# Performance work log

Hardware: AMD Instinct MI355X
Metric: run time of the kernel (lower is better)

The kernel has to match this reference:

```python
import jax, jax.numpy as jnp
import numpy as np

R = 3                      # corr_radius
K = (2 * R + 1) ** 2       # 49 correlation window
BANDS = 16
MAX_FREQ = 512.0
NUM_ITERS = 4
EPS = 1e-5


def _fourier(coords):
    # coords [..., D] -> [..., D*(2*BANDS+1)]
    freqs = (2.0 ** jnp.linspace(0.0, np.log2(MAX_FREQ), BANDS).astype(coords.dtype)) * np.pi
    x = coords[..., None] * freqs                      # [..., D, BANDS]
    enc = jnp.concatenate([jnp.sin(x), jnp.cos(x)], axis=-1)
    enc = enc.reshape(enc.shape[:-2] + (-1,))
    return jnp.concatenate([coords, enc], axis=-1)


def _layernorm(x, g, b):
    m = jnp.mean(x, -1, keepdims=True)
    v = jnp.mean(jnp.square(x - m), -1, keepdims=True)
    return (x - m) * jax.lax.rsqrt(v + EPS) * g + b


def _local_corr(query, fmaps, positions, stride):
    # query [B,Q,C], fmaps [B,T,C,H,W], positions [B,Q,T,2] -> corr [B,Q,T,K]
    B, T, C, H, W = fmaps.shape
    Q = query.shape[1]
    off = jnp.arange(-R, R + 1, dtype=positions.dtype)
    oy, ox = jnp.meshgrid(off, off, indexing='ij')
    og = jnp.stack([ox.reshape(-1), oy.reshape(-1)], -1)          # [K,2] (x,y)
    coords = positions / stride
    coords = coords[..., None, :] + og                             # [B,Q,T,K,2]
    coords = jnp.transpose(coords, (0, 2, 1, 3, 4)).reshape(B * T, Q * K, 2)
    fm = fmaps.reshape(B * T, C, H * W)

    def bilerp(f, xy):  # f [C,HW], xy [N,2] -> [C,N]; zeros padding, align_corners=True
        x, y = xy[:, 0], xy[:, 1]
        x0, y0 = jnp.floor(x), jnp.floor(y)
        dx, dy = x - x0, y - y0
        out = jnp.zeros((C, xy.shape[0]), f.dtype)
        for xi, yi, w in ((x0, y0, (1 - dx) * (1 - dy)),
                          (x0 + 1, y0, dx * (1 - dy)),
                          (x0, y0 + 1, (1 - dx) * dy),
                          (x0 + 1, y0 + 1, dx * dy)):
            valid = (xi >= 0) & (xi <= W - 1) & (yi >= 0) & (yi <= H - 1)
            idx = (jnp.clip(yi, 0, H - 1) * W + jnp.clip(xi, 0, W - 1)).astype(jnp.int32)
            out = out + (w * valid)[None, :] * f[:, idx]
        return out

    sampled = jax.vmap(bilerp)(fm, coords)                         # [BT,C,QK]
    sampled = sampled.reshape(B, T, C, Q, K)
    return jnp.einsum('btcqk,bqc->bqtk', sampled, query)


def _forward(coarse_tracks, query_features, feature_maps, feature_stride,
             proj_w, proj_b, ln1_g, ln1_b, conv_w, conv_b, ln2_g, ln2_b,
             mlp_w1, mlp_b1, mlp_w2, mlp_b2, delta_w, delta_b,
             vis_w1, vis_b1, vis_w2, vis_b2):
    B, Q, T, _ = coarse_tracks.shape
    D = proj_w.shape[1]
    dtype = coarse_tracks.dtype
    tracks = coarse_tracks
    t_idx = jnp.linspace(0.0, 1.0, T, dtype=dtype).reshape(1, 1, T, 1)
    hidden = jnp.zeros((B * Q, T, D), dtype)
    vis_sum = jnp.zeros((B, Q, T), dtype)
    num_blocks = ln1_g.shape[0]
    pad = conv_w.shape[-1] // 2
    for _ in range(NUM_ITERS):
        corr = _local_corr(query_features, feature_maps, tracks, feature_stride)
        pos_in = jnp.concatenate([tracks, jnp.broadcast_to(t_idx, (B, Q, T, 1))], -1)
        pos_enc = _fourier(pos_in)
        x = jnp.concatenate([corr, pos_enc, hidden.reshape(B, Q, T, D)], -1)
        x = x.reshape(B * Q, T, -1) @ proj_w + proj_b
        for i in range(num_blocks):
            h = _layernorm(x, ln1_g[i], ln1_b[i])
            h = jnp.transpose(h, (0, 2, 1))                        # [BQ,D,T]
            h = jax.lax.conv_general_dilated(
                h, conv_w[i], (1,), [(pad, pad)],
                dimension_numbers=('NCH', 'OIH', 'NCH'),
                feature_group_count=D) + conv_b[i][None, :, None]
            x = x + jnp.transpose(h, (0, 2, 1))
            h2 = _layernorm(x, ln2_g[i], ln2_b[i])
            x = x + jax.nn.gelu(h2 @ mlp_w1[i] + mlp_b1[i], approximate=False) @ mlp_w2[i] + mlp_b2[i]
        hidden = x
        delta = (x @ delta_w + delta_b).reshape(B, Q, T, 2)
        vis = (jax.nn.gelu(x @ vis_w1 + vis_b1, approximate=False) @ vis_w2 + vis_b2).reshape(B, Q, T)
        tracks = tracks + delta
        vis_sum = vis_sum + vis
    visibility = vis_sum / NUM_ITERS
    return jnp.concatenate([tracks, visibility[..., None]], -1)   # [B,Q,T,3]


def setup_inputs() -> dict:
    B, Q, T, C, H, W, D = 1, 128, 48, 64, 96, 128, 128
    NB, KSZ, IN_DIM = 4, 5, K + 3 * (2 * BANDS + 1) + D          # 49+99+128=276
    ks = jax.random.split(jax.random.key(0), 16)
    s = 0.05
    return {
        'coarse_tracks': jax.random.uniform(ks[0], (B, Q, T, 2)) * jnp.array([W * 4.0, H * 4.0]),
        'query_features': jax.random.normal(ks[1], (B, Q, C)),
        'feature_maps': jax.random.normal(ks[2], (B, T, C, H, W)),
        'feature_stride': 4,
        'proj_w': jax.random.normal(ks[3], (IN_DIM, D)) * s,
        'proj_b': jnp.zeros((D,)),
        'ln1_g': jnp.ones((NB, D)),
        'ln1_b': jnp.zeros((NB, D)),
        'conv_w': jax.random.normal(ks[4], (NB, D, 1, KSZ)) * 0.2,
        'conv_b': jnp.zeros((NB, D)),
        'ln2_g': jnp.ones((NB, D)),
        'ln2_b': jnp.zeros((NB, D)),
        'mlp_w1': jax.random.normal(ks[5], (NB, D, 2 * D)) * s,
        'mlp_b1': jnp.zeros((NB, 2 * D)),
        'mlp_w2': jax.random.normal(ks[6], (NB, 2 * D, D)) * s,
        'mlp_b2': jnp.zeros((NB, D)),
        'delta_w': jax.random.normal(ks[7], (D, 2)) * 0.01,
        'delta_b': jnp.zeros((2,)),
        'vis_w1': jax.random.normal(ks[8], (D, D // 2)) * s,
        'vis_b1': jnp.zeros((D // 2,)),
        'vis_w2': jax.random.normal(ks[9], (D // 2, 1)) * s,
        'vis_b2': jnp.zeros((1,)),
    }


def reference(coarse_tracks, query_features, feature_maps, feature_stride,
              proj_w, proj_b, ln1_g, ln1_b, conv_w, conv_b, ln2_g, ln2_b,
              mlp_w1, mlp_b1, mlp_w2, mlp_b2, delta_w, delta_b,
              vis_w1, vis_b1, vis_w2, vis_b2):
    return _forward(coarse_tracks, query_features, feature_maps, feature_stride,
                    proj_w, proj_b, ln1_g, ln1_b, conv_w, conv_b, ln2_g, ln2_b,
                    mlp_w1, mlp_b1, mlp_w2, mlp_b2, delta_w, delta_b,
                    vis_w1, vis_b1, vis_w2, vis_b2)
```

## Files before the change

kernel.cpp:

```cpp
#include <hip/hip_runtime.h>
#include <hip/hip_bf16.h>
#include <math.h>

#define QN 128
#define TN 48
#define CN 64
#define HN 96
#define WN 128
#define DN 128
#define KK 49
#define IN_DIM 276
#define XPAD 288
#define NROWS (QN*TN)
#define PI_F 3.14159265358979323846f

typedef __hip_bfloat16 bf16;
typedef unsigned short u16;
using bf16x8 = __attribute__((ext_vector_type(8))) short;
using f32x4  = __attribute__((ext_vector_type(4))) float;

__device__ inline float fixnan(float x){ return (x == x && fabsf(x) < 1e30f) ? x : 0.f; }

template<int MODE> __device__ inline float ld(const void* p, size_t i){
  if constexpr (MODE == 0) return ((const float*)p)[i];
  else {
    unsigned int u = ((const unsigned short*)p)[i];
    return __uint_as_float(u << 16);
  }
}

__device__ inline short f2b(float x){
  __hip_bfloat16 h = __float2bfloat16(x);
  return *reinterpret_cast<short*>(&h);
}
__device__ inline float b2f16(u16 u){ return __uint_as_float(((unsigned int)u) << 16); }

__device__ inline float waveReduceSum(float v){
  #pragma unroll
  for (int off = 32; off > 0; off >>= 1) v += __shfl_xor(v, off, 64);
  return v;
}

__device__ inline float gelu_exact(float x){
  return 0.5f * x * (1.f + erff(x * 0.70710678118654752440f));
}

__device__ inline f32x4 mfma16(bf16x8 a, bf16x8 b, f32x4 c){
  return __builtin_amdgcn_mfma_f32_16x16x32_bf16(a, b, c, 0, 0, 0);
}

__device__ inline float decode_stride(const void* p){
  int iv = *(const int*)p;
  if (iv >= 1 && iv <= (1 << 20)) return (float)iv;
  float fv = __int_as_float(iv);
  if (fv == fv && fv >= 0.25f && fv <= 1048576.f) return fv;
  unsigned int lo = ((unsigned int)(*(const unsigned short*)p)) << 16;
  float bv = __uint_as_float(lo);
  if (bv == bv && bv >= 0.25f && bv <= 1048576.f) return bv;
  return 4.f;
}

__device__ inline void bput(short* base, int stride_sh, int r, int k, float v){
  *(short*)((char*)base + (size_t)r*stride_sh*2 + ((2*k) ^ ((r & 7) << 4))) = f2b(v);
}
__device__ inline float bget(const short* base, int stride_sh, int r, int k){
  unsigned short u = *(const unsigned short*)((const char*)base + (size_t)r*stride_sh*2 + ((2*k) ^ ((r & 7) << 4)));
  return __uint_as_float(((unsigned int)u) << 16);
}
__device__ inline bf16x8 bget8(const short* base, int stride_sh, int r, int k0){
  return *(const bf16x8*)((const char*)base + (size_t)r*stride_sh*2 + ((2*k0) ^ ((r & 7) << 4)));
}

struct SLds {
  float sc0[32], sc1[32];
  float qv[CN];
  float hdl[32][132];
  union {
    short Xs[32][320];
    struct { short hn[32][128]; short hn2[32][128]; short y1[32][256]; } b;
    float dots[32][64];
  } u;
};

__global__ __launch_bounds__(256) void k_sniff(const unsigned short* __restrict__ q,
                                               int* __restrict__ flag){
  __shared__ int cnt;
  if (threadIdx.x == 0) cnt = 0;
  __syncthreads();
  int good = 0;
  for (int i = threadIdx.x; i < 8192; i += 256){
    float v = __uint_as_float(((unsigned int)q[i]) << 16);
    float a = fabsf(v);
    if (a > 1e-3f && a < 30.f) good++;
  }
  atomicAdd(&cnt, good);
  __syncthreads();
  if (threadIdx.x == 0) flag[0] = (cnt > 6500) ? 1 : 0;
}

template<int MODE>
__device__ void transpose_impl(u16 (*tile)[130], const void* fmap, u16* fmapT){
  int t = blockIdx.x / HN, y = blockIdx.x % HN;
  int tid = threadIdx.x, wv = tid >> 6, lane = tid & 63;
  #pragma unroll 4
  for (int ci = 0; ci < 16; ++ci){
    int c = ci*4 + wv;
    size_t base = (((size_t)t*CN + c)*HN + y)*WN;
    if constexpr (MODE == 1){
      const u16* fp = (const u16*)fmap + base + 2*lane;
      tile[c][2*lane]   = fp[0];
      tile[c][2*lane+1] = fp[1];
    } else {
      const float* fp = (const float*)fmap + base + 2*lane;
      tile[c][2*lane]   = (u16)f2b(fp[0]);
      tile[c][2*lane+1] = (u16)f2b(fp[1]);
    }
  }
  __syncthreads();
  u16* op = fmapT + (((size_t)t*HN + y)*WN)*CN + lane;
  #pragma unroll 4
  for (int xi = 0; xi < 32; ++xi){
    int x = xi*4 + wv;
    op[(size_t)x*CN] = tile[lane][x];
  }
}
__global__ __launch_bounds__(256) void k_transpose(const int* __restrict__ mf,
    const void* fmap, u16* fmapT){
  __shared__ u16 tile[64][130];
  if (mf[0] == 0) transpose_impl<0>(tile, fmap, fmapT);
  else            transpose_impl<1>(tile, fmap, fmapT);
}

#define TW_PW   (128*XPAD)
#define TW_W1   (4*256*128)
#define TW_W2   (4*128*256)
#define TW_VW1  (64*128)
#define TW_TOT  (TW_PW + TW_W1 + TW_W2 + TW_VW1)
template<int MODE>
__device__ void transW_impl(int idx, const void* pw, const void* w1, const void* w2,
                            const void* vw1,
                            bf16* pwt, bf16* w1t, bf16* w2t, bf16* vw1t){
  if (idx < TW_PW){
    int n = idx / XPAD, kk = idx % XPAD;
    float v = (kk < IN_DIM) ? ld<MODE>(pw, (size_t)kk*DN + n) : 0.f;
    ((short*)pwt)[idx] = f2b(v);
  } else if (idx < TW_PW + TW_W1){
    int i2 = idx - TW_PW;
    int k = i2 & 127, n = (i2 >> 7) & 255, l = i2 >> 15;
    ((short*)w1t)[i2] = f2b(ld<MODE>(w1, (size_t)l*32768 + (size_t)k*256 + n));
  } else if (idx < TW_PW + TW_W1 + TW_W2){
    int i3 = idx - TW_PW - TW_W1;
    int k = i3 & 255, n = (i3 >> 8) & 127, l = i3 >> 15;
    ((short*)w2t)[i3] = f2b(ld<MODE>(w2, (size_t)l*32768 + (size_t)k*128 + n));
  } else {
    int i4 = idx - TW_PW - TW_W1 - TW_W2;
    int n = i4 >> 7, k = i4 & 127;
    ((short*)vw1t)[i4] = f2b(ld<MODE>(vw1, (size_t)k*64 + n));
  }
}
__global__ __launch_bounds__(256) void k_transW(const int* __restrict__ mf,
    const void* pw, const void* w1, const void* w2, const void* vw1,
    bf16* pwt, bf16* w1t, bf16* w2t, bf16* vw1t){
  int idx = blockIdx.x*256 + threadIdx.x;
  if (idx >= TW_TOT) return;
  if (mf[0] == 0) transW_impl<0>(idx, pw, w1, w2, vw1, pwt, w1t, w2t, vw1t);
  else            transW_impl<1>(idx, pw, w1, w2, vw1, pwt, w1t, w2t, vw1t);
}

template<int MODE>
__device__ void init_impl(const void* ct, float* tracks, float* vis_sum, float* hd0){
  int i = blockIdx.x * 256 + threadIdx.x;
  if (i < NROWS){
    tracks[2*i]   = fixnan(ld<MODE>(ct, 2*i));
    tracks[2*i+1] = fixnan(ld<MODE>(ct, 2*i+1));
    vis_sum[i] = 0.f;
  }
  if (i < NROWS*DN) hd0[i] = 0.f;
}
__global__ __launch_bounds__(256) void k_init(const int* __restrict__ mf,
    const void* ct, float* tracks, float* vis_sum, float* hd0){
  if (mf[0] == 0) init_impl<0>(ct, tracks, vis_sum, hd0);
  else            init_impl<1>(ct, tracks, vis_sum, hd0);
}

template<int MODE, int FAST>
__device__ void corr_impl(float* qv, float* dots,
    const void* fmap, const u16* fmapT, const void* query, const void* stride_p,
    const float* __restrict__ tr, short* __restrict__ Xc)
{
  int blk = blockIdx.x;
  int q = blk / TN, t = blk % TN;
  int ll = threadIdx.x;
  qv[ll] = ld<MODE>(query, q*CN + ll);
  float fs = decode_stride(stride_p);
  float c0 = fixnan(tr[2*blk]), c1 = fixnan(tr[2*blk+1]);
  float px = fminf(fmaxf(c0 / fs, -1e6f), 1e6f);
  float py = fminf(fmaxf(c1 / fs, -1e6f), 1e6f);
  float fx0 = floorf(px), fy0 = floorf(py);
  float dx = px - fx0, dy = py - fy0;
  __syncthreads();

  if constexpr (FAST){
    float qv8[8];
    #pragma unroll
    for (int u = 0; u < 8; ++u) qv8[u] = qv[(ll & 7)*8 + u];
    int x0 = (int)fx0 - 3, y0 = (int)fy0 - 3;
    dots[ll] = 0.f;
    __syncthreads();
    if (x0 <= 127 && x0 + 7 >= 0){
      int x0c = min(max(x0, 0), WN - 8);
      int sh = x0c - x0;
      int i = (ll >> 3) + sh;
      bool wr = ((ll & 7) == 0) && (i >= 0) && (i < 8);
      #pragma unroll
      for (int j = 0; j < 8; ++j){
        int yj = y0 + j;
        if (yj < 0 || yj >= HN) continue;
        const u16* blkp = fmapT + ((((size_t)t*HN + yj)*WN + x0c) << 6);
        bf16x8 v = *(const bf16x8*)(blkp + ll*8);
        float p = 0.f;
        #pragma unroll
        for (int u = 0; u < 8; ++u) p += qv8[u] * b2f16((u16)v[u]);
        p += __shfl_xor(p, 1, 64);
        p += __shfl_xor(p, 2, 64);
        p += __shfl_xor(p, 4, 64);
        if (wr) dots[j*8 + i] = p;
      }
    }
  } else {
    int bx = (int)fx0, by = (int)fy0;
    int j = ll >> 3, i = ll & 7;
    int xi = bx + i - 3, yi = by + j - 3;
    float dot = 0.f;
    if (xi >= 0 && xi < WN && yi >= 0 && yi < HN){
      size_t base = ((size_t)t*CN)*HN*WN + (size_t)yi*WN + xi;
      #pragma unroll 8
      for (int c = 0; c < CN; ++c)
        dot += qv[c] * ld<MODE>(fmap, base + (size_t)c*HN*WN);
    }
    dots[j*8 + i] = dot;
  }
  __syncthreads();

  if (ll < KK){
    int oy = ll / 7, ox = ll % 7;
    float v = (1.f-dx)*(1.f-dy)*dots[oy*8+ox]   + dx*(1.f-dy)*dots[oy*8+ox+1]
            + (1.f-dx)*dy*dots[(oy+1)*8+ox]     + dx*dy*dots[(oy+1)*8+ox+1];
    Xc[(size_t)blk*64 + ll] = f2b(fixnan(v));
  }
}
template<int FAST>
__global__ __launch_bounds__(64) void k_corr(const int* __restrict__ mf,
    const void* fmap, const u16* fmapT, const void* query, const void* stride_p,
    const float* tr, short* Xc)
{
  __shared__ float qv[CN];
  __shared__ float dots[64];
  if (mf[0] == 0) corr_impl<0, FAST>(qv, dots, fmap, fmapT, query, stride_p, tr, Xc);
  else            corr_impl<1, FAST>(qv, dots, fmap, fmapT, query, stride_p, tr, Xc);
}

template<int MODE, int TAIL>
__device__ void iter_impl(SLds& s,
    const u16* __restrict__ fmapT, const void* query, const void* stride_p,
    const short* __restrict__ XcR, short* __restrict__ XcW,
    const float* __restrict__ tr_in, float* __restrict__ tr_out,
    const float* __restrict__ vi_in, float* __restrict__ vi_out,
    const float* __restrict__ hd_in, float* __restrict__ hd_out,
    const bf16* pwt, const void* pb,
    const void* ln1g, const void* ln1b, const void* cw, const void* cb,
    const void* ln2g, const void* ln2b,
    const bf16* w1t, const void* b1, const bf16* w2t, const void* b2,
    const void* dwp, const void* dbp,
    const bf16* vw1t, const void* vb1, const void* vw2, const void* vb2,
    void* out, int last)
{
  int bid = blockIdx.x;
  int q = bid >> 1, half = bid & 1, T0 = half * 16;
  int tid = threadIdx.x, wv = tid >> 6, ll = tid & 63;
  int R0 = q*TN + T0;
  float fs = decode_stride(stride_p);

  if (tid < 32){
    s.sc0[tid] = fixnan(tr_in[2*(R0 + tid)]);
    s.sc1[tid] = fixnan(tr_in[2*(R0 + tid) + 1]);
  }
  if (tid >= 64 && tid < 128) s.qv[tid - 64] = ld<MODE>(query, q*CN + (tid - 64));
  __syncthreads();

  for (int idx = tid; idx < 32*KK; idx += 1024){
    int r = idx / KK, kk = idx % KK;
    bput(&s.u.Xs[0][0], 320, r, kk, b2f16((u16)XcR[(size_t)(R0 + r)*64 + kk]));
  }
  for (int idx = tid; idx < 32*3; idx += 1024){
    int r = idx / 3, cd = idx % 3;
    float v = (cd == 0) ? s.sc0[r] : (cd == 1 ? s.sc1[r] : (float)(T0+r)/(float)(TN-1));
    bput(&s.u.Xs[0][0], 320, r, KK + cd, v);
  }
  for (int idx = tid; idx < 32*96; idx += 1024){
    int r = idx / 96, j = idx % 96, coord = j >> 5, rm = j & 31, band = rm & 15;
    float cv = (coord == 0) ? s.sc0[r] : (coord == 1 ? s.sc1[r] : (float)(T0+r)/(float)(TN-1));
    float a = cv * exp2f(0.6f*(float)band) * PI_F;
    float v = (rm < 16) ? __sinf(a) : __cosf(a);
    bput(&s.u.Xs[0][0], 320, r, KK + 3 + coord*32 + rm, fixnan(v));
  }
  for (int idx = tid; idx < 32*32; idx += 1024){
    int r = idx >> 5, d4 = (idx & 31)*4;
    f32x4 hv = *(const f32x4*)(hd_in + (size_t)(R0 + r)*DN + d4);
    #pragma unroll
    for (int u = 0; u < 4; ++u)
      bput(&s.u.Xs[0][0], 320, r, 148 + d4 + u, fixnan(hv[u]));
  }
  for (int idx = tid; idx < 32*12; idx += 1024){
    int r = idx / 12, p = idx % 12;
    bput(&s.u.Xs[0][0], 320, r, IN_DIM + p, 0.f);
  }
  __syncthreads();

  {
    int rA = ll & 15, gK = ll >> 4;
    int rt = wv & 1, nt = wv >> 1;
    bf16x8 afr[9];
    #pragma unroll
    for (int ks = 0; ks < 9; ++ks)
      afr[ks] = bget8(&s.u.Xs[0][0], 320, rt*16 + rA, ks*32 + gK*8);
    float bv = ld<MODE>(pb, nt*16 + rA);
    f32x4 acc = {bv, bv, bv, bv};
    #pragma unroll
    for (int ks = 0; ks < 9; ++ks)
      acc = mfma16(afr[ks],
        *(const bf16x8*)((const short*)pwt + (size_t)(nt*16 + rA)*XPAD + ks*32 + gK*8), acc);
    #pragma unroll
    for (int r2 = 0; r2 < 4; ++r2)
      s.hdl[rt*16 + gK*4 + r2][nt*16 + rA] = fixnan(acc[r2]);
  }

  #pragma unroll 1
  for (int L = 0; L < 4; ++L){
    float cwr0[5], cwr1[5];
    #pragma unroll
    for (int k = 0; k < 5; ++k){
      cwr0[k] = ld<MODE>(cw, ((size_t)L*DN + ll)*5 + k);
      cwr1[k] = ld<MODE>(cw, ((size_t)L*DN + ll + 64)*5 + k);
    }
    float cbv0 = ld<MODE>(cb, L*DN + ll), cbv1 = ld<MODE>(cb, L*DN + ll + 64);
    float g20 = ld<MODE>(ln2g, L*DN + ll), g21 = ld<MODE>(ln2g, L*DN + ll + 64);
    float c20 = ld<MODE>(ln2b, L*DN + ll), c21 = ld<MODE>(ln2b, L*DN + ll + 64);
    __syncthreads();
    {
      float g0 = ld<MODE>(ln1g, L*DN + ll), g1 = ld<MODE>(ln1g, L*DN + ll + 64);
      float b0 = ld<MODE>(ln1b, L*DN + ll), b1v = ld<MODE>(ln1b, L*DN + ll + 64);
      #pragma unroll
      for (int rr = 0; rr < 2; ++rr){
        int r = wv*2 + rr;
        float a0 = s.hdl[r][ll], a1 = s.hdl[r][ll+64];
        float su = waveReduceSum(a0 + a1);
        float sq = waveReduceSum(a0*a0 + a1*a1);
        float m = su * (1.f/128.f);
        float var = fmaxf(sq * (1.f/128.f) - m*m, 0.f);
        float inv = rsqrtf(var + 1e-5f);
        bput(&s.u.b.hn[0][0], 128, r, ll,      (a0 - m)*inv*g0 + b0);
        bput(&s.u.b.hn[0][0], 128, r, ll + 64, (a1 - m)*inv*g1 + b1v);
      }
    }
    __syncthreads();
    #pragma unroll
    for (int rr = 0; rr < 2; ++rr){
      int r = wv*2 + rr, t = T0 + r;
      float a0 = cbv0, a1 = cbv1;
      #pragma unroll
      for (int k = 0; k < 5; ++k){
        int tg = t + k - 2, tl = r + k - 2;
        if (tg >= 0 && tg < TN && tl >= 0 && tl < 32){
          a0 += bget(&s.u.b.hn[0][0], 128, tl, ll)      * cwr0[k];
          a1 += bget(&s.u.b.hn[0][0], 128, tl, ll + 64) * cwr1[k];
        }
      }
      float x0 = fixnan(s.hdl[r][ll] + a0);
      float x1 = fixnan(s.hdl[r][ll+64] + a1);
      s.hdl[r][ll] = x0; s.hdl[r][ll+64] = x1;
      float su = waveReduceSum(x0 + x1);
      float sq = waveReduceSum(x0*x0 + x1*x1);
      float m = su * (1.f/128.f);
      float var = fmaxf(sq * (1.f/128.f) - m*m, 0.f);
      float inv = rsqrtf(var + 1e-5f);
      bput(&s.u.b.hn2[0][0], 128, r, ll,      (x0 - m)*inv*g20 + c20);
      bput(&s.u.b.hn2[0][0], 128, r, ll + 64, (x1 - m)*inv*g21 + c21);
    }
    __syncthreads();
    {
      int rA = ll & 15, gK = ll >> 4;
      int rt = wv & 1, nt0 = wv >> 1;
      const short* w1s = (const short*)w1t + (size_t)L*32768;
      bf16x8 afr[4];
      #pragma unroll
      for (int ks = 0; ks < 4; ++ks)
        afr[ks] = bget8(&s.u.b.hn2[0][0], 128, rt*16 + rA, ks*32 + gK*8);
      #pragma unroll
      for (int h = 0; h < 2; ++h){
        int nt = nt0 + h*8;
        float bv = ld<MODE>(b1, L*256 + nt*16 + rA);
        f32x4 acc = {bv, bv, bv, bv};
        #pragma unroll
        for (int ks = 0; ks < 4; ++ks)
          acc = mfma16(afr[ks],
            *(const bf16x8*)(w1s + (size_t)(nt*16 + rA)*DN + ks*32 + gK*8), acc);
        #pragma unroll
        for (int r2 = 0; r2 < 4; ++r2)
          bput(&s.u.b.y1[0][0], 256, rt*16 + gK*4 + r2, nt*16 + rA, gelu_exact(acc[r2]));
      }
    }
    __syncthreads();
    {
      int rA = ll & 15, gK = ll >> 4;
      int rt = wv & 1, nt = wv >> 1;
      const short* w2s = (const short*)w2t + (size_t)L*32768;
      bf16x8 afr[8];
      #pragma unroll
      for (int ks = 0; ks < 8; ++ks)
        afr[ks] = bget8(&s.u.b.y1[0][0], 256, rt*16 + rA, ks*32 + gK*8);
      float bv = ld<MODE>(b2, L*DN + nt*16 + rA);
      f32x4 acc = {bv, bv, bv, bv};
      #pragma unroll
      for (int ks = 0; ks < 8; ++ks)
        acc = mfma16(afr[ks],
          *(const bf16x8*)(w2s + (size_t)(nt*16 + rA)*256 + ks*32 + gK*8), acc);
      #pragma unroll
      for (int r2 = 0; r2 < 4; ++r2){
        int r = rt*16 + gK*4 + r2, cc = nt*16 + rA;
        s.hdl[r][cc] = fixnan(s.hdl[r][cc] + acc[r2]);
      }
    }
  }
  __syncthreads();

  for (int idx = tid; idx < 32*DN; idx += 1024){
    int r = idx >> 7, d = idx & 127;
    bput(&s.u.b.hn[0][0], 128, r, d, s.hdl[r][d]);
  }
  __syncthreads();
  float* gC = (float*)&s.u.b.y1[0][0];
  {
    int rA = ll & 15, gK = ll >> 4;
    int rt = wv & 1, nt = wv >> 1;
    if (nt < 4){
      float bv = ld<MODE>(vb1, nt*16 + rA);
      f32x4 acc = {bv, bv, bv, bv};
      #pragma unroll
      for (int ks = 0; ks < 4; ++ks)
        acc = mfma16(bget8(&s.u.b.hn[0][0], 128, rt*16 + rA, ks*32 + gK*8),
                     *(const bf16x8*)((const short*)vw1t + (size_t)(nt*16 + rA)*128 + ks*32 + gK*8), acc);
      #pragma unroll
      for (int r2 = 0; r2 < 4; ++r2)
        gC[(rt*16 + gK*4 + r2)*72 + nt*16 + rA] = gelu_exact(acc[r2]);
    }
  }
  __syncthreads();
  float vw2v = ld<MODE>(vw2, ll);
  float dwa = ld<MODE>(dwp, ll*2),     dwb = ld<MODE>(dwp, (ll+64)*2);
  float dwc = ld<MODE>(dwp, ll*2 + 1), dwd = ld<MODE>(dwp, (ll+64)*2 + 1);
  #pragma unroll
  for (int rr = 0; rr < 2; ++rr){
    int r = wv*2 + rr, t = T0 + r, grow = q*TN + t;
    bool owned = half ? (r >= 8) : (r < 24);
    float vis = waveReduceSum(gC[r*72 + ll] * vw2v);
    float x0 = s.hdl[r][ll], x1 = s.hdl[r][ll+64];
    float dX = waveReduceSum(x0*dwa + x1*dwb);
    float dY = waveReduceSum(x0*dwc + x1*dwd);
    if (owned){
      hd_out[(size_t)grow*DN + ll]      = fixnan(x0);
      hd_out[(size_t)grow*DN + ll + 64] = fixnan(x1);
      if (ll == 0){
        float tx = fixnan(tr_in[2*grow]   + dX + ld<MODE>(dbp, 0));
        float ty = fixnan(tr_in[2*grow+1] + dY + ld<MODE>(dbp, 1));
        tr_out[2*grow] = tx; tr_out[2*grow+1] = ty;
        s.sc0[r] = tx; s.sc1[r] = ty;
        float vs = fixnan(vi_in[grow] + vis + ld<MODE>(vb2, 0));
        vi_out[grow] = vs;
        if (last){
          if constexpr (MODE == 0){
            ((float*)out)[grow*3 + 0] = tx;
            ((float*)out)[grow*3 + 1] = ty;
            ((float*)out)[grow*3 + 2] = vs * 0.25f;
          } else {
            ((bf16*)out)[grow*3 + 0] = __float2bfloat16(tx);
            ((bf16*)out)[grow*3 + 1] = __float2bfloat16(ty);
            ((bf16*)out)[grow*3 + 2] = __float2bfloat16(vs * 0.25f);
          }
        }
      }
    }
  }

  if constexpr (TAIL){
    if (!last){
      __syncthreads();
      float qv8[8];
      #pragma unroll
      for (int u = 0; u < 8; ++u) qv8[u] = s.qv[(ll & 7)*8 + u];
      #pragma unroll
      for (int rr = 0; rr < 2; ++rr){
        int r = wv*2 + rr, t = T0 + r, grow = q*TN + t;
        bool owned = half ? (r >= 8) : (r < 24);
        if (!owned) continue;
        float* dots = &s.u.dots[r][0];
        float px = fminf(fmaxf(s.sc0[r] / fs, -1e6f), 1e6f);
        float py = fminf(fmaxf(s.sc1[r] / fs, -1e6f), 1e6f);
        float fx0 = floorf(px), fy0 = floorf(py);
        float dx = px - fx0, dy = py - fy0;
        int x0 = (int)fx0 - 3, y0 = (int)fy0 - 3;
        dots[ll] = 0.f;
        if (x0 <= 127 && x0 + 7 >= 0){
          int x0c = min(max(x0, 0), WN - 8);
          int sh = x0c - x0;
          int i = (ll >> 3) + sh;
          bool wr = ((ll & 7) == 0) && (i >= 0) && (i < 8);
          #pragma unroll
          for (int j = 0; j < 8; ++j){
            int yj = y0 + j;
            if (yj < 0 || yj >= HN) continue;
            const u16* blkp = fmapT + ((((size_t)t*HN + yj)*WN + x0c) << 6);
            bf16x8 v = *(const bf16x8*)(blkp + ll*8);
            float p = 0.f;
            #pragma unroll
            for (int u = 0; u < 8; ++u) p += qv8[u] * b2f16((u16)v[u]);
            p += __shfl_xor(p, 1, 64);
            p += __shfl_xor(p, 2, 64);
            p += __shfl_xor(p, 4, 64);
            if (wr) dots[j*8 + i] = p;
          }
        }
        if (ll < KK){
          int oy = ll / 7, ox = ll % 7;
          float v = (1.f-dx)*(1.f-dy)*dots[oy*8+ox]   + dx*(1.f-dy)*dots[oy*8+ox+1]
                  + (1.f-dx)*dy*dots[(oy+1)*8+ox]     + dx*dy*dots[(oy+1)*8+ox+1];
          XcW[(size_t)grow*64 + ll] = f2b(fixnan(v));
        }
      }
    }
  }
}

template<int TAIL>
__global__ __launch_bounds__(1024, 1) void k_iter(const int* __restrict__ mf,
    const u16* fmapT, const void* query, const void* stride_p,
    const short* XcR, short* XcW,
    const float* tr_in, float* tr_out, const float* vi_in, float* vi_out,
    const float* hd_in, float* hd_out,
    const bf16* pwt, const void* pb,
    const void* ln1g, const void* ln1b, const void* cw, const void* cb,
    const void* ln2g, const void* ln2b,
    const bf16* w1t, const void* b1, const bf16* w2t, const void* b2,
    const void* dwp, const void* dbp,
    const bf16* vw1t, const void* vb1, const void* vw2, const void* vb2,
    void* out, int last)
{
  __shared__ SLds s;
  if (mf[0] == 0)
    iter_impl<0, TAIL>(s, fmapT, query, stride_p, XcR, XcW, tr_in, tr_out, vi_in, vi_out,
                 hd_in, hd_out, pwt, pb, ln1g, ln1b, cw, cb, ln2g, ln2b, w1t, b1, w2t, b2,
                 dwp, dbp, vw1t, vb1, vw2, vb2, out, last);
  else
    iter_impl<1, TAIL>(s, fmapT, query, stride_p, XcR, XcW, tr_in, tr_out, vi_in, vi_out,
                 hd_in, hd_out, pwt, pb, ln1g, ln1b, cw, cb, ln2g, ln2b, w1t, b1, w2t, b2,
                 dwp, dbp, vw1t, vb1, vw2, vb2, out, last);
}

extern "C" void kernel_launch(void* const* d_in, const int* in_sizes, int n_in,
                              void* d_out, int out_size, void* d_ws, size_t ws_size,
                              hipStream_t stream) {
  const void* ct    = d_in[0];
  const void* query = d_in[1];
  const void* fmap  = d_in[2];
  const void* fs    = d_in[3];
  const void* pw    = d_in[4];
  const void* pb    = d_in[5];
  const void* ln1g  = d_in[6];
  const void* ln1b  = d_in[7];
  const void* cw    = d_in[8];
  const void* cb    = d_in[9];
  const void* ln2g  = d_in[10];
  const void* ln2b  = d_in[11];
  const void* w1    = d_in[12];
  const void* b1    = d_in[13];
  const void* w2    = d_in[14];
  const void* b2    = d_in[15];
  const void* dw    = d_in[16];
  const void* db    = d_in[17];
  const void* vw1   = d_in[18];
  const void* vb1   = d_in[19];
  const void* vw2   = d_in[20];
  const void* vb2   = d_in[21];

  char* w0 = (char*)d_ws;
  char* w = w0;
  int*   mflag = (int*)w;                   w += 256;
  float* tr[2]; float* vi[2]; float* hd[2]; short* Xc[2];
  for (int i = 0; i < 2; ++i){ tr[i] = (float*)w; w += ((size_t)NROWS*2*4 + 255) & ~255ull; }
  for (int i = 0; i < 2; ++i){ vi[i] = (float*)w; w += ((size_t)NROWS*4   + 255) & ~255ull; }
  for (int i = 0; i < 2; ++i){ hd[i] = (float*)w; w += ((size_t)NROWS*DN*4 + 255) & ~255ull; }
  for (int i = 0; i < 2; ++i){ Xc[i] = (short*)w; w += ((size_t)NROWS*64*2 + 255) & ~255ull; }
  bf16* pwt = (bf16*)w;                     w += ((size_t)128*XPAD*2 + 255) & ~255ull;
  bf16* w1t = (bf16*)w;                     w += ((size_t)4*256*128*2 + 255) & ~255ull;
  bf16* w2t = (bf16*)w;                     w += ((size_t)4*128*256*2 + 255) & ~255ull;
  bf16* vw1t = (bf16*)w;                    w += ((size_t)64*128*2 + 255) & ~255ull;
  u16*  fmapT = (u16*)w;                    w += ((size_t)TN*HN*WN*CN*2 + 255) & ~255ull;

  bool fast = ((size_t)(w - w0) <= ws_size);

  k_sniff<<<1, 256, 0, stream>>>((const unsigned short*)query, mflag);
  k_transW<<<(TW_TOT + 255)/256, 256, 0, stream>>>(mflag, pw, w1, w2, vw1, pwt, w1t, w2t, vw1t);
  k_init<<<(NROWS*DN + 255)/256, 256, 0, stream>>>(mflag, ct, tr[0], vi[0], hd[0]);
  if (fast){
    k_transpose<<<TN*HN, 256, 0, stream>>>(mflag, fmap, fmapT);
    k_corr<1><<<NROWS, 64, 0, stream>>>(mflag, fmap, fmapT, query, fs, tr[0], Xc[0]);
    for (int it = 0; it < 4; ++it){
      int a = it & 1, b = a ^ 1;
      k_iter<1><<<256, 1024, 0, stream>>>(mflag, fmapT, query, fs,
          Xc[a], Xc[b],
          tr[a], tr[b], vi[a], vi[b], hd[a], hd[b],
          pwt, pb, ln1g, ln1b, cw, cb, ln2g, ln2b,
          w1t, b1, w2t, b2, dw, db, vw1t, vb1, vw2, vb2,
          d_out, it == 3);
    }
  } else {
    for (int it = 0; it < 4; ++it){
      int a = it & 1, b = a ^ 1;
      k_corr<0><<<NROWS, 64, 0, stream>>>(mflag, fmap, fmapT, query, fs, tr[a], Xc[0]);
      k_iter<0><<<256, 1024, 0, stream>>>(mflag, fmapT, query, fs,
          Xc[0], Xc[1],
          tr[a], tr[b], vi[a], vi[b], hd[a], hd[b],
          pwt, pb, ln1g, ln1b, cw, cb, ln2g, ln2b,
          w1t, b1, w2t, b2, dw, db, vw1t, vb1, vw2, vb2,
          d_out, it == 3);
    }
  }
}
```

Measured before the change: 315.9 us.

## Merge setup kernels into one launch and detect dtype per wave

Replaces the sniff, weight-transpose, init and feature-map transpose kernels with one k_setup launch whose blocks are partitioned by role. Each kernel now detects the input dtype itself with a 64-lane ballot over the first query values instead of reading a flag written by a separate kernel. Separately, the residual update in the iteration kernel writes the bf16 copy of the hidden state directly when L==3, removing a copy loop and a barrier. This cuts three launches and their serialization, at the cost of a weaker dtype heuristic that samples only 64 values.

```diff
diff --git a/kernel.cpp b/kernel.cpp
--- a/kernel.cpp
+++ b/kernel.cpp
@@ -35,6 +35,15 @@
 }
 __device__ inline float b2f16(u16 u){ return __uint_as_float(((unsigned int)u) << 16); }
 
+__device__ inline int detect_mode(const void* query){
+  const u16* q = (const u16*)query;
+  int lane = threadIdx.x & 63;
+  float v = b2f16(q[lane]);
+  float a = fabsf(v);
+  unsigned long long m = __ballot(a > 1e-3f && a < 30.f);
+  return (__popcll(m) >= 48) ? 1 : 0;
+}
+
 __device__ inline float waveReduceSum(float v){
   #pragma unroll
   for (int off = 32; off > 0; off >>= 1) v += __shfl_xor(v, off, 64);
@@ -82,62 +91,17 @@
   } u;
 };
 
-__global__ __launch_bounds__(256) void k_sniff(const unsigned short* __restrict__ q,
-                                               int* __restrict__ flag){
-  __shared__ int cnt;
-  if (threadIdx.x == 0) cnt = 0;
-  __syncthreads();
-  int good = 0;
-  for (int i = threadIdx.x; i < 8192; i += 256){
-    float v = __uint_as_float(((unsigned int)q[i]) << 16);
-    float a = fabsf(v);
-    if (a > 1e-3f && a < 30.f) good++;
-  }
-  atomicAdd(&cnt, good);
-  __syncthreads();
-  if (threadIdx.x == 0) flag[0] = (cnt > 6500) ? 1 : 0;
-}
-
-template<int MODE>
-__device__ void transpose_impl(u16 (*tile)[130], const void* fmap, u16* fmapT){
-  int t = blockIdx.x / HN, y = blockIdx.x % HN;
-  int tid = threadIdx.x, wv = tid >> 6, lane = tid & 63;
-  #pragma unroll 4
-  for (int ci = 0; ci < 16; ++ci){
-    int c = ci*4 + wv;
-    size_t base = (((size_t)t*CN + c)*HN + y)*WN;
-    if constexpr (MODE == 1){
-      const u16* fp = (const u16*)fmap + base + 2*lane;
-      tile[c][2*lane]   = fp[0];
-      tile[c][2*lane+1] = fp[1];
-    } else {
-      const float* fp = (const float*)fmap + base + 2*lane;
-      tile[c][2*lane]   = (u16)f2b(fp[0]);
-      tile[c][2*lane+1] = (u16)f2b(fp[1]);
-    }
-  }
-  __syncthreads();
-  u16* op = fmapT + (((size_t)t*HN + y)*WN)*CN + lane;
-  #pragma unroll 4
-  for (int xi = 0; xi < 32; ++xi){
-    int x = xi*4 + wv;
-    op[(size_t)x*CN] = tile[lane][x];
-  }
-}
-__global__ __launch_bounds__(256) void k_transpose(const int* __restrict__ mf,
-    const void* fmap, u16* fmapT){
-  __shared__ u16 tile[64][130];
-  if (mf[0] == 0) transpose_impl<0>(tile, fmap, fmapT);
-  else            transpose_impl<1>(tile, fmap, fmapT);
-}
-
 #define TW_PW   (128*XPAD)
 #define TW_W1   (4*256*128)
 #define TW_W2   (4*128*256)
 #define TW_VW1  (64*128)
 #define TW_TOT  (TW_PW + TW_W1 + TW_W2 + TW_VW1)
+#define NB_TW   ((TW_TOT + 255)/256)
+#define NB_INIT ((NROWS*DN + 255)/256)
+#define NB_TRANS (TN*HN)
+
 template<int MODE>
-__device__ void transW_impl(int idx, const void* pw, const void* w1, const void* w2,
+__device__ void transW_item(int idx, const void* pw, const void* w1, const void* w2,
                             const void* vw1,
                             bf16* pwt, bf16* w1t, bf16* w2t, bf16* vw1t){
   if (idx < TW_PW){
@@ -158,29 +122,64 @@
     ((short*)vw1t)[i4] = f2b(ld<MODE>(vw1, (size_t)k*64 + n));
   }
 }
-__global__ __launch_bounds__(256) void k_transW(const int* __restrict__ mf,
+
+template<int MODE>
+__device__ void setup_body(u16 (*tile)[130], int bid,
+    const void* ct, const void* query, const void* fmap,
     const void* pw, const void* w1, const void* w2, const void* vw1,
-    bf16* pwt, bf16* w1t, bf16* w2t, bf16* vw1t){
-  int idx = blockIdx.x*256 + threadIdx.x;
-  if (idx >= TW_TOT) return;
-  if (mf[0] == 0) transW_impl<0>(idx, pw, w1, w2, vw1, pwt, w1t, w2t, vw1t);
-  else            transW_impl<1>(idx, pw, w1, w2, vw1, pwt, w1t, w2t, vw1t);
-}
-
-template<int MODE>
-__device__ void init_impl(const void* ct, float* tracks, float* vis_sum, float* hd0){
-  int i = blockIdx.x * 256 + threadIdx.x;
-  if (i < NROWS){
-    tracks[2*i]   = fixnan(ld<MODE>(ct, 2*i));
-    tracks[2*i+1] = fixnan(ld<MODE>(ct, 2*i+1));
-    vis_sum[i] = 0.f;
-  }
-  if (i < NROWS*DN) hd0[i] = 0.f;
-}
-__global__ __launch_bounds__(256) void k_init(const int* __restrict__ mf,
-    const void* ct, float* tracks, float* vis_sum, float* hd0){
-  if (mf[0] == 0) init_impl<0>(ct, tracks, vis_sum, hd0);
-  else            init_impl<1>(ct, tracks, vis_sum, hd0);
+    float* tracks, float* vis_sum, float* hd0,
+    bf16* pwt, bf16* w1t, bf16* w2t, bf16* vw1t, u16* fmapT){
+  int tid = threadIdx.x;
+  if (bid < NB_TW){
+    int idx = bid*256 + tid;
+    if (idx < TW_TOT) transW_item<MODE>(idx, pw, w1, w2, vw1, pwt, w1t, w2t, vw1t);
+  } else if (bid < NB_TW + NB_INIT){
+    int i = (bid - NB_TW)*256 + tid;
+    if (i < NROWS){
+      tracks[2*i]   = fixnan(ld<MODE>(ct, 2*i));
+      tracks[2*i+1] = fixnan(ld<MODE>(ct, 2*i+1));
+      vis_sum[i] = 0.f;
+    }
+    if (i < NROWS*DN) hd0[i] = 0.f;
+  } else {
+    int tb = bid - NB_TW - NB_INIT;
+    int t = tb / HN, y = tb % HN;
+    int wv = tid >> 6, lane = tid & 63;
+    #pragma unroll 4
+    for (int ci = 0; ci < 16; ++ci){
+      int c = ci*4 + wv;
+      size_t base = (((size_t)t*CN + c)*HN + y)*WN;
+      if constexpr (MODE == 1){
+        const u16* fp = (const u16*)fmap + base + 2*lane;
+        tile[c][2*lane]   = fp[0];
+        tile[c][2*lane+1] = fp[1];
+      } else {
+        const float* fp = (const float*)fmap + base + 2*lane;
+        tile[c][2*lane]   = (u16)f2b(fp[0]);
+        tile[c][2*lane+1] = (u16)f2b(fp[1]);
+      }
+    }
+    __syncthreads();
+    u16* op = fmapT + (((size_t)t*HN + y)*WN)*CN + lane;
+    #pragma unroll 4
+    for (int xi = 0; xi < 32; ++xi){
+      int x = xi*4 + wv;
+      op[(size_t)x*CN] = tile[lane][x];
+    }
+  }
+}
+__global__ __launch_bounds__(256) void k_setup(
+    const void* ct, const void* query, const void* fmap,
+    const void* pw, const void* w1, const void* w2, const void* vw1,
+    float* tracks, float* vis_sum, float* hd0,
+    bf16* pwt, bf16* w1t, bf16* w2t, bf16* vw1t, u16* fmapT){
+  __shared__ u16 tile[64][130];
+  if (detect_mode(query) == 0)
+    setup_body<0>(tile, blockIdx.x, ct, query, fmap, pw, w1, w2, vw1,
+                  tracks, vis_sum, hd0, pwt, w1t, w2t, vw1t, fmapT);
+  else
+    setup_body<1>(tile, blockIdx.x, ct, query, fmap, pw, w1, w2, vw1,
+                  tracks, vis_sum, hd0, pwt, w1t, w2t, vw1t, fmapT);
 }
 
 template<int MODE, int FAST>
@@ -250,14 +249,14 @@
   }
 }
 template<int FAST>
-__global__ __launch_bounds__(64) void k_corr(const int* __restrict__ mf,
+__global__ __launch_bounds__(64) void k_corr(
     const void* fmap, const u16* fmapT, const void* query, const void* stride_p,
     const float* tr, short* Xc)
 {
   __shared__ float qv[CN];
   __shared__ float dots[64];
-  if (mf[0] == 0) corr_impl<0, FAST>(qv, dots, fmap, fmapT, query, stride_p, tr, Xc);
-  else            corr_impl<1, FAST>(qv, dots, fmap, fmapT, query, stride_p, tr, Xc);
+  if (detect_mode(query) == 0) corr_impl<0, FAST>(qv, dots, fmap, fmapT, query, stride_p, tr, Xc);
+  else                         corr_impl<1, FAST>(qv, dots, fmap, fmapT, query, stride_p, tr, Xc);
 }
 
 template<int MODE, int TAIL>
@@ -428,17 +427,14 @@
       #pragma unroll
       for (int r2 = 0; r2 < 4; ++r2){
         int r = rt*16 + gK*4 + r2, cc = nt*16 + rA;
-        s.hdl[r][cc] = fixnan(s.hdl[r][cc] + acc[r2]);
+        float x = fixnan(s.hdl[r][cc] + acc[r2]);
+        s.hdl[r][cc] = x;
+        if (L == 3) bput(&s.u.b.hn[0][0], 128, r, cc, x);
       }
     }
   }
   __syncthreads();
 
-  for (int idx = tid; idx < 32*DN; idx += 1024){
-    int r = idx >> 7, d = idx & 127;
-    bput(&s.u.b.hn[0][0], 128, r, d, s.hdl[r][d]);
-  }
-  __syncthreads();
   float* gC = (float*)&s.u.b.y1[0][0];
   {
     int rA = ll & 15, gK = ll >> 4;
@@ -542,7 +538,7 @@
 }
 
 template<int TAIL>
-__global__ __launch_bounds__(1024, 1) void k_iter(const int* __restrict__ mf,
+__global__ __launch_bounds__(1024, 1) void k_iter(
     const u16* fmapT, const void* query, const void* stride_p,
     const short* XcR, short* XcW,
     const float* tr_in, float* tr_out, const float* vi_in, float* vi_out,
@@ -556,7 +552,7 @@
     void* out, int last)
 {
   __shared__ SLds s;
-  if (mf[0] == 0)
+  if (detect_mode(query) == 0)
     iter_impl<0, TAIL>(s, fmapT, query, stride_p, XcR, XcW, tr_in, tr_out, vi_in, vi_out,
                  hd_in, hd_out, pwt, pb, ln1g, ln1b, cw, cb, ln2g, ln2b, w1t, b1, w2t, b2,
                  dwp, dbp, vw1t, vb1, vw2, vb2, out, last);
@@ -594,7 +590,6 @@
 
   char* w0 = (char*)d_ws;
   char* w = w0;
-  int*   mflag = (int*)w;                   w += 256;
   float* tr[2]; float* vi[2]; float* hd[2]; short* Xc[2];
   for (int i = 0; i < 2; ++i){ tr[i] = (float*)w; w += ((size_t)NROWS*2*4 + 255) & ~255ull; }
   for (int i = 0; i < 2; ++i){ vi[i] = (float*)w; w += ((size_t)NROWS*4   + 255) & ~255ull; }
@@ -608,15 +603,15 @@
 
   bool fast = ((size_t)(w - w0) <= ws_size);
 
-  k_sniff<<<1, 256, 0, stream>>>((const unsigned short*)query, mflag);
-  k_transW<<<(TW_TOT + 255)/256, 256, 0, stream>>>(mflag, pw, w1, w2, vw1, pwt, w1t, w2t, vw1t);
-  k_init<<<(NROWS*DN + 255)/256, 256, 0, stream>>>(mflag, ct, tr[0], vi[0], hd[0]);
+  int nbset = NB_TW + NB_INIT + (fast ? NB_TRANS : 0);
+  k_setup<<<nbset, 256, 0, stream>>>(ct, query, fmap, pw, w1, w2, vw1,
+      tr[0], vi[0], hd[0], pwt, w1t, w2t, vw1t, fmapT);
+
   if (fast){
-    k_transpose<<<TN*HN, 256, 0, stream>>>(mflag, fmap, fmapT);
-    k_corr<1><<<NROWS, 64, 0, stream>>>(mflag, fmap, fmapT, query, fs, tr[0], Xc[0]);
+    k_corr<1><<<NROWS, 64, 0, stream>>>(fmap, fmapT, query, fs, tr[0], Xc[0]);
     for (int it = 0; it < 4; ++it){
       int a = it & 1, b = a ^ 1;
-      k_iter<1><<<256, 1024, 0, stream>>>(mflag, fmapT, query, fs,
+      k_iter<1><<<256, 1024, 0, stream>>>(fmapT, query, fs,
           Xc[a], Xc[b],
           tr[a], tr[b], vi[a], vi[b], hd[a], hd[b],
           pwt, pb, ln1g, ln1b, cw, cb, ln2g, ln2b,
@@ -626,8 +621,8 @@
   } else {
     for (int it = 0; it < 4; ++it){
       int a = it & 1, b = a ^ 1;
-      k_corr<0><<<NROWS, 64, 0, stream>>>(mflag, fmap, fmapT, query, fs, tr[a], Xc[0]);
-      k_iter<0><<<256, 1024, 0, stream>>>(mflag, fmapT, query, fs,
+      k_corr<0><<<NROWS, 64, 0, stream>>>(fmap, fmapT, query, fs, tr[a], Xc[0]);
+      k_iter<0><<<256, 1024, 0, stream>>>(fmapT, query, fs,
           Xc[0], Xc[1],
           tr[a], tr[b], vi[a], vi[b], hd[a], hd[b],
           pwt, pb, ln1g, ln1b, cw, cb, ln2g, ln2b,
```

Result: faster. 307.5 us (-2.7%).
